# Kernel tuning notes

Hardware: AMD Instinct MI355X
Metric: run time of the kernel (lower is better)

Reference implementation:

```python
import jax, jax.numpy as jnp
import numpy as np

B, C, S, H, W = 2, 192, 16, 32, 32
NH, P = 6, 4          # num_heads, n_points (n_points hardcoded = 4 in source)
HD = C // NH          # head_dim = 32
HID = 4 * C           # mlp hidden (mlp_ratio = 4.0)
L = S * H * W
EPS = 1e-5


def _offset_bias():
    # Faithful to DeformAttention._reset_parameters grid init.
    thetas = np.arange(NH, dtype=np.float32) * (2.0 * np.pi / NH)
    g = np.stack([np.cos(thetas), np.sin(thetas) * np.cos(thetas), np.sin(thetas) * np.sin(thetas)], -1)
    g = g / np.abs(g).max(-1, keepdims=True)
    g = np.tile(g[:, None, :], (1, P, 1)).copy()
    for i in range(P):
        g[:, i, :] *= (i + 1)
    return jnp.asarray(g.reshape(-1), dtype=jnp.float32)


def setup_inputs() -> dict:
    key = jax.random.key(0)
    ks = jax.random.split(key, 8)
    w = lambda k, shp, s: jax.random.normal(k, shp, jnp.float32) * s
    return {
        "x": jax.random.normal(ks[0], (B, C, S, H, W), jnp.float32),
        "mask_matrix": 0,  # unused (shift_size == 0)
        "Wv": w(ks[1], (C, C), C ** -0.5), "bv": jnp.zeros((C,), jnp.float32),
        "Woff": w(ks[2], (C, NH * P * 3), 0.01), "boff": _offset_bias(),
        "Waw": w(ks[3], (C, NH * P), 0.02), "baw": jnp.zeros((NH * P,), jnp.float32),
        "Wout": w(ks[4], (C, C), C ** -0.5), "bout": jnp.zeros((C,), jnp.float32),
        "g2": jnp.ones((C,), jnp.float32), "b2": jnp.zeros((C,), jnp.float32),
        "W1": w(ks[5], (C, HID), C ** -0.5), "b1": jnp.zeros((HID,), jnp.float32),
        "W2": w(ks[6], (HID, C), HID ** -0.5), "b2m": jnp.zeros((C,), jnp.float32),
    }


def _layernorm(x, g, b):
    m = jnp.mean(x, -1, keepdims=True)
    v = jnp.mean(jnp.square(x - m), -1, keepdims=True)
    return (x - m) * jax.lax.rsqrt(v + EPS) * g + b


def _ref_points():
    # get_reference_points with valid_ratios == 1 (mask_ is all-zeros in source).
    d = (jnp.arange(S, dtype=jnp.float32) + 0.5) / S
    y = (jnp.arange(H, dtype=jnp.float32) + 0.5) / H
    x = (jnp.arange(W, dtype=jnp.float32) + 0.5) / W
    rd, ry, rx = jnp.meshgrid(d, y, x, indexing="ij")
    # stacked as (d, x, y), matching normalizer (D, W, H)
    return jnp.stack([rd.reshape(-1), rx.reshape(-1), ry.reshape(-1)], -1)  # (L, 3)


def _deform_core(value, loc, aw):
    # value: (B,L,NH,HD); loc: (B,L,NH,P,3) in [0,1] as (d,x,y); aw: (B,L,NH,P)
    v = value.transpose(0, 2, 1, 3)  # (B,NH,L,HD), L flattened as d*H*W + y*W + x
    pd = loc[..., 0] * S - 0.5  # align_corners=False pixel coords
    px = loc[..., 1] * W - 0.5
    py = loc[..., 2] * H - 0.5
    d0f, x0f, y0f = jnp.floor(pd), jnp.floor(px), jnp.floor(py)
    fd, fx, fy = pd - d0f, px - x0f, py - y0f
    d0, x0, y0 = d0f.astype(jnp.int32), x0f.astype(jnp.int32), y0f.astype(jnp.int32)
    acc = jnp.zeros((B, NH, L * P, HD), value.dtype)
    for dd in (0, 1):
        for dy in (0, 1):
            for dx in (0, 1):
                di, yi, xi = d0 + dd, y0 + dy, x0 + dx
                wgt = (fd if dd else 1.0 - fd) * (fy if dy else 1.0 - fy) * (fx if dx else 1.0 - fx)
                inb = (di >= 0) & (di < S) & (yi >= 0) & (yi < H) & (xi >= 0) & (xi < W)
                idx = (jnp.clip(di, 0, S - 1) * H + jnp.clip(yi, 0, H - 1)) * W + jnp.clip(xi, 0, W - 1)
                idx = idx.transpose(0, 2, 1, 3).reshape(B, NH, L * P)
                samp = jnp.take_along_axis(v, idx[..., None], axis=2)  # (B,NH,L*P,HD)
                wz = jnp.where(inb, wgt, 0.0).transpose(0, 2, 1, 3).reshape(B, NH, L * P, 1)
                acc = acc + samp * wz
    acc = acc.reshape(B, NH, L, P, HD)
    out = jnp.sum(acc * aw.transpose(0, 2, 1, 3)[..., None], axis=3)  # (B,NH,L,HD)
    return out.transpose(0, 2, 1, 3).reshape(B, L, NH * HD)


def reference(x, mask_matrix, Wv, bv, Woff, boff, Waw, baw, Wout, bout, g2, b2, W1, b1, W2, b2m):
    # shortcut = x.view(B, S*H*W, C) on channel-first memory (faithful to source view)
    shortcut = x.reshape(B, L, C)
    xp = x.transpose(0, 2, 3, 4, 1).reshape(B, L, C)  # token-major layout used by attn

    # DeformAttention
    value = (xp @ Wv + bv).reshape(B, L, NH, HD)
    off = (xp @ Woff + boff).reshape(B, L, NH, P, 3)
    aw = jax.nn.softmax((xp @ Waw + baw).reshape(B, L, NH, P), axis=-1)
    norm = jnp.array([S, W, H], jnp.float32)
    loc = _ref_points()[None, :, None, None, :] + off / norm  # (B,L,NH,P,3)
    attn = _deform_core(value, loc, aw) @ Wout + bout  # (B,L,C)

    h = shortcut + attn
    h = h + (jax.nn.gelu(_layernorm(h, g2, b2) @ W1 + b1, approximate=False) @ W2 + b2m)
    return h.reshape(B, S, H, W, C).transpose(0, 4, 1, 2, 3)  # (B,C,S,H,W)
```

## Files before the change

### kernel.cpp

```cpp
#include <hip/hip_runtime.h>
#include <hip/hip_bf16.h>
#include <math.h>

#define BB 2
#define CC 192
#define SS 16
#define HH 32
#define WW 32
#define NH 6
#define PP 4
#define HD 32
#define HID 768
#define LL (SS * HH * WW)
#define MTOK (BB * LL)
#define NPROJ 288

typedef unsigned short u16;
typedef u16 u16x8 __attribute__((ext_vector_type(8)));
typedef __bf16 bf16x8 __attribute__((ext_vector_type(8)));
typedef float f32x4 __attribute__((ext_vector_type(4)));

static __device__ __forceinline__ u16 f2b(float f) {
    __hip_bfloat16 h = __float2bfloat16(f);
    return *reinterpret_cast<u16*>(&h);
}

static __device__ __forceinline__ float fast_gelu(float v) {
    float z = 1.5957691216057308f * (v + 0.044715f * v * v * v);
    return v * __builtin_amdgcn_rcpf(1.0f + __expf(-z));
}

__global__ void build_weights(const float* __restrict__ Wv, const float* __restrict__ Woff,
                              const float* __restrict__ Waw, const float* __restrict__ Wout,
                              const float* __restrict__ W1, const float* __restrict__ W2,
                              const float* __restrict__ bv, const float* __restrict__ boff,
                              const float* __restrict__ baw,
                              u16* __restrict__ wcatT, u16* __restrict__ woutT,
                              u16* __restrict__ w1T, u16* __restrict__ w2T,
                              float* __restrict__ bcat) {
    int i = blockIdx.x * 256 + threadIdx.x;
    if (i < NPROJ * CC) {
        int n = i / CC, k = i % CC;
        float v = (n < 192) ? Wv[k * 192 + n]
                : (n < 264) ? Woff[k * 72 + (n - 192)]
                            : Waw[k * 24 + (n - 264)];
        wcatT[i] = f2b(v);
        return;
    }
    i -= NPROJ * CC;
    if (i < CC * CC) {
        int n = i / CC, k = i % CC;
        woutT[i] = f2b(Wout[k * CC + n]);
        return;
    }
    i -= CC * CC;
    if (i < HID * CC) {
        int n = i / CC, k = i % CC;
        w1T[i] = f2b(W1[k * HID + n]);
        return;
    }
    i -= HID * CC;
    if (i < CC * HID) {
        int n = i / HID, k = i % HID;
        w2T[i] = f2b(W2[k * CC + n]);
        return;
    }
    i -= CC * HID;
    if (i < NPROJ) {
        float v = (i < 192) ? bv[i] : (i < 264) ? boff[i - 192] : baw[i - 264];
        bcat[i] = v;
    }
}

__global__ void transpose_in(const float* __restrict__ x, u16* __restrict__ xp) {
    __shared__ float s[32][33];
    int b = blockIdx.z;
    int c0 = blockIdx.y * 32;
    int l0 = blockIdx.x * 32;
    int tx = threadIdx.x, ty = threadIdx.y;
#pragma unroll
    for (int r = 0; r < 32; r += 8)
        s[ty + r][tx] = x[((size_t)b * CC + c0 + ty + r) * LL + l0 + tx];
    __syncthreads();
#pragma unroll
    for (int r = 0; r < 32; r += 8)
        xp[((size_t)b * LL + l0 + ty + r) * CC + c0 + tx] = f2b(s[tx][ty + r]);
}

template<int EPI, int NF>
__global__ __launch_bounds__(256, 2) void gemm_mfma(const u16* __restrict__ A,
                                                    const u16* __restrict__ Bt,
                                                    const float* __restrict__ bias,
                                                    const float* __restrict__ add,
                                                    void* __restrict__ Cout,
                                                    void* __restrict__ Cout2,
                                                    int M, int N, int K) {
    constexpr int BN = NF * 32;
    __shared__ u16 As[128][40];
    __shared__ u16 Bs[BN][40];
    int t = threadIdx.x;
    int m0 = blockIdx.y * 128;
    int n0 = blockIdx.x * BN;
    int w = t >> 6, lane = t & 63;
    int wm = w >> 1, wn = w & 1;
    int lrow = lane & 15, q = lane >> 4;
    int lk8 = q * 8;

    f32x4 acc[4][NF];
#pragma unroll
    for (int i = 0; i < 4; ++i)
#pragma unroll
        for (int f = 0; f < NF; ++f)
#pragma unroll
            for (int r = 0; r < 4; ++r) acc[i][f][r] = 0.f;

    int arow = t >> 2, aseg = (t & 3) * 8;

    for (int k0 = 0; k0 < K; k0 += 32) {
        *reinterpret_cast<u16x8*>(&As[arow][aseg]) =
            *reinterpret_cast<const u16x8*>(A + (size_t)(m0 + arow) * K + k0 + aseg);
        *reinterpret_cast<u16x8*>(&As[arow + 64][aseg]) =
            *reinterpret_cast<const u16x8*>(A + (size_t)(m0 + arow + 64) * K + k0 + aseg);
#pragma unroll
        for (int idx = 0; idx < BN * 4; idx += 256) {
            int ii = idx + t;
            if (ii < BN * 4) {
                int br = ii >> 2, bseg = (ii & 3) * 8;
                *reinterpret_cast<u16x8*>(&Bs[br][bseg]) =
                    *reinterpret_cast<const u16x8*>(Bt + (size_t)(n0 + br) * K + k0 + bseg);
            }
        }
        __syncthreads();
        bf16x8 af[4], bfr[NF];
#pragma unroll
        for (int i = 0; i < 4; ++i)
            af[i] = *reinterpret_cast<const bf16x8*>(&As[wm * 64 + i * 16 + lrow][lk8]);
#pragma unroll
        for (int f = 0; f < NF; ++f)
            bfr[f] = *reinterpret_cast<const bf16x8*>(&Bs[wn * (16 * NF) + f * 16 + lrow][lk8]);
#pragma unroll
        for (int i = 0; i < 4; ++i)
#pragma unroll
            for (int f = 0; f < NF; ++f) {
                if (EPI == 3)
                    acc[i][f] = __builtin_amdgcn_mfma_f32_16x16x32_bf16(af[i], bfr[f], acc[i][f], 0, 0, 0);
                else
                    acc[i][f] = __builtin_amdgcn_mfma_f32_16x16x32_bf16(bfr[f], af[i], acc[i][f], 0, 0, 0);
            }
        __syncthreads();
    }

    if (EPI == 3) {
#pragma unroll
        for (int i = 0; i < 4; ++i) {
#pragma unroll
            for (int f = 0; f < NF; ++f) {
                int n = n0 + wn * (16 * NF) + f * 16 + lrow;
                float bvn = bias[n];
                int mb = m0 + wm * 64 + i * 16 + q * 4;
                float4 vv;
#pragma unroll
                for (int r = 0; r < 4; ++r)
                    ((float*)&vv)[r] = acc[i][f][r] + bvn + add[(size_t)(mb + r) * N + n];
                int b = mb >> 14, l = mb & (LL - 1);
                *reinterpret_cast<float4*>((float*)Cout + ((size_t)b * CC + n) * LL + l) = vv;
            }
        }
    } else {
#pragma unroll
        for (int i = 0; i < 4; ++i) {
            int m = m0 + wm * 64 + i * 16 + lrow;
#pragma unroll
            for (int f = 0; f < NF; ++f) {
                int nq = n0 + wn * (16 * NF) + f * 16 + q * 4;
                float4 bias4 = *reinterpret_cast<const float4*>(bias + nq);
                if (EPI == 0) {
                    if (nq < 192) {
                        int h = nq >> 5, hd = nq & 31;
                        int b = m >> 14, l = m & (LL - 1);
                        u16 p0 = f2b(acc[i][f][0] + bias4.x);
                        u16 p1 = f2b(acc[i][f][1] + bias4.y);
                        u16 p2 = f2b(acc[i][f][2] + bias4.z);
                        u16 p3 = f2b(acc[i][f][3] + bias4.w);
                        uint2 pk = make_uint2((unsigned)p0 | ((unsigned)p1 << 16),
                                              (unsigned)p2 | ((unsigned)p3 << 16));
                        *reinterpret_cast<uint2*>(
                            (u16*)Cout + (((size_t)b * NH + h) * LL + l) * HD + hd) = pk;
                    } else {
                        float4 vv;
                        vv.x = acc[i][f][0] + bias4.x;
                        vv.y = acc[i][f][1] + bias4.y;
                        vv.z = acc[i][f][2] + bias4.z;
                        vv.w = acc[i][f][3] + bias4.w;
                        *reinterpret_cast<float4*>((float*)Cout2 + (size_t)m * 96 + (nq - 192)) = vv;
                    }
                } else if (EPI == 1) {
                    float4 add4 = *reinterpret_cast<const float4*>(add + (size_t)m * N + nq);
                    float4 vv;
                    vv.x = acc[i][f][0] + bias4.x + add4.x;
                    vv.y = acc[i][f][1] + bias4.y + add4.y;
                    vv.z = acc[i][f][2] + bias4.z + add4.z;
                    vv.w = acc[i][f][3] + bias4.w + add4.w;
                    *reinterpret_cast<float4*>((float*)Cout + (size_t)m * N + nq) = vv;
                } else {
                    u16 p0 = f2b(fast_gelu(acc[i][f][0] + bias4.x));
                    u16 p1 = f2b(fast_gelu(acc[i][f][1] + bias4.y));
                    u16 p2 = f2b(fast_gelu(acc[i][f][2] + bias4.z));
                    u16 p3 = f2b(fast_gelu(acc[i][f][3] + bias4.w));
                    uint2 pk = make_uint2((unsigned)p0 | ((unsigned)p1 << 16),
                                          (unsigned)p2 | ((unsigned)p3 << 16));
                    *reinterpret_cast<uint2*>((u16*)Cout + (size_t)m * N + nq) = pk;
                }
            }
        }
    }
}

__global__ __launch_bounds__(256) void deform_kernel(const u16* __restrict__ vbuf,
                                                     const float* __restrict__ offaw,
                                                     u16* __restrict__ dout) {
    __shared__ uint2 cw[8][32];
    int gl = threadIdx.x >> 5;
    int g = blockIdx.x * 8 + gl;
    int j = threadIdx.x & 31;
    int h = g % NH;
    int tmp = g / NH;
    int l = tmp % LL;
    int b = tmp / LL;
    int d = l >> 10, rem = l & 1023, y = rem >> 5, xw = rem & 31;

    const float* oa = offaw + (size_t)(b * LL + l) * 96;
    int p = j >> 3, cor = j & 7;
    int dx = cor & 1, dy = (cor >> 1) & 1, dd = cor >> 2;

    float4 lg = *reinterpret_cast<const float4*>(oa + 72 + h * 4);
    float mx = fmaxf(fmaxf(lg.x, lg.y), fmaxf(lg.z, lg.w));
    float e0 = __expf(lg.x - mx), e1 = __expf(lg.y - mx);
    float e2 = __expf(lg.z - mx), e3 = __expf(lg.w - mx);
    float inv = __builtin_amdgcn_rcpf(e0 + e1 + e2 + e3);
    float ep = (p == 0) ? e0 : (p == 1) ? e1 : (p == 2) ? e2 : e3;
    float awp = ep * inv;

    const float* op = oa + (h * 4 + p) * 3;
    float pd = (d + 0.5f) + op[0] - 0.5f;
    float px = (xw + 0.5f) + op[1] - 0.5f;
    float py = (y + 0.5f) + op[2] - 0.5f;
    float d0f = floorf(pd), x0f = floorf(px), y0f = floorf(py);
    float fd = pd - d0f, fx = px - x0f, fy = py - y0f;
    int di = (int)d0f + dd, yi = (int)y0f + dy, xi = (int)x0f + dx;
    bool inb = (di >= 0) & (di < SS) & (yi >= 0) & (yi < HH) & (xi >= 0) & (xi < WW);
    float wgt = (dd ? fd : 1.f - fd) * (dy ? fy : 1.f - fy) * (dx ? fx : 1.f - fx) * awp;
    wgt = inb ? wgt : 0.f;
    int dic = min(max(di, 0), SS - 1);
    int yic = min(max(yi, 0), HH - 1);
    int xic = min(max(xi, 0), WW - 1);
    int bo = (((dic * HH) + yic) * WW + xic) * (HD * 2);

    cw[gl][j] = make_uint2((unsigned)bo, __float_as_uint(wgt));
    __syncthreads();

    const char* vhead = (const char*)(vbuf + ((size_t)(b * NH + h) * LL) * HD) + 2 * j;
    const uint4* cw4 = reinterpret_cast<const uint4*>(&cw[gl][0]);
    float acc = 0.f;
#pragma unroll
    for (int qq = 0; qq < 16; ++qq) {
        uint4 c = cw4[qq];
        u16 v0 = *reinterpret_cast<const u16*>(vhead + c.x);
        u16 v1 = *reinterpret_cast<const u16*>(vhead + c.z);
        acc += __uint_as_float(c.y) * __uint_as_float(((unsigned)v0) << 16);
        acc += __uint_as_float(c.w) * __uint_as_float(((unsigned)v1) << 16);
    }
    dout[(size_t)(b * LL + l) * CC + h * HD + j] = f2b(acc);
}

__global__ __launch_bounds__(256) void layernorm_kernel(const float* __restrict__ hin,
                                                        const float* __restrict__ g2,
                                                        const float* __restrict__ b2,
                                                        u16* __restrict__ lnout) {
    int row = blockIdx.x * 4 + (threadIdx.x >> 6);
    int lane = threadIdx.x & 63;
    const float* hr = hin + (size_t)row * CC;
    float v0 = hr[lane], v1 = hr[lane + 64], v2 = hr[lane + 128];
    float s = v0 + v1 + v2;
    float sq = v0 * v0 + v1 * v1 + v2 * v2;
#pragma unroll
    for (int o = 32; o > 0; o >>= 1) {
        s += __shfl_xor(s, o);
        sq += __shfl_xor(sq, o);
    }
    float m = s * (1.0f / CC);
    float var = sq * (1.0f / CC) - m * m;
    float r = rsqrtf(var + 1e-5f);
    u16* lo = lnout + (size_t)row * CC;
    lo[lane]       = f2b((v0 - m) * r * g2[lane]       + b2[lane]);
    lo[lane + 64]  = f2b((v1 - m) * r * g2[lane + 64]  + b2[lane + 64]);
    lo[lane + 128] = f2b((v2 - m) * r * g2[lane + 128] + b2[lane + 128]);
}

extern "C" void kernel_launch(void* const* d_in, const int* in_sizes, int n_in,
                              void* d_out, int out_size, void* d_ws, size_t ws_size,
                              hipStream_t stream) {
    const float* x    = (const float*)d_in[0];
    const float* Wv   = (const float*)d_in[2];
    const float* bv   = (const float*)d_in[3];
    const float* Woff = (const float*)d_in[4];
    const float* boff = (const float*)d_in[5];
    const float* Waw  = (const float*)d_in[6];
    const float* baw  = (const float*)d_in[7];
    const float* Wout = (const float*)d_in[8];
    const float* bout = (const float*)d_in[9];
    const float* g2   = (const float*)d_in[10];
    const float* b2   = (const float*)d_in[11];
    const float* W1   = (const float*)d_in[12];
    const float* b1   = (const float*)d_in[13];
    const float* W2   = (const float*)d_in[14];
    const float* b2m  = (const float*)d_in[15];

    char* wsb = (char*)d_ws;
    u16*   xp    = (u16*)(wsb + 0);
    u16*   vbuf  = (u16*)(wsb + 12582912);
    float* offaw = (float*)(wsb + 25165824);
    u16*   dbuf  = (u16*)(wsb + 0);
    u16*   hid   = (u16*)(wsb + 12582912);
    float* hbuf  = (float*)(wsb + 66060288);
    u16*   ln    = (u16*)(wsb + 92274688);
    u16*   wcatT = (u16*)(wsb + 105906176);
    u16*   woutT = wcatT + NPROJ * CC;
    u16*   w1T   = woutT + CC * CC;
    u16*   w2T   = w1T + HID * CC;
    float* bcat  = (float*)(w2T + CC * HID);
    float* out   = (float*)d_out;

    int wtot = NPROJ * CC + CC * CC + HID * CC + CC * HID + NPROJ;
    build_weights<<<(wtot + 255) / 256, 256, 0, stream>>>(
        Wv, Woff, Waw, Wout, W1, W2, bv, boff, baw, wcatT, woutT, w1T, w2T, bcat);
    transpose_in<<<dim3(LL / 32, CC / 32, BB), dim3(32, 8), 0, stream>>>(x, xp);
    gemm_mfma<0, 3><<<dim3(3, MTOK / 128), 256, 0, stream>>>(
        xp, wcatT, bcat, nullptr, vbuf, offaw, MTOK, NPROJ, CC);
    deform_kernel<<<(BB * LL * NH) / 8, 256, 0, stream>>>(vbuf, offaw, dbuf);
    gemm_mfma<1, 3><<<dim3(2, MTOK / 128), 256, 0, stream>>>(
        dbuf, woutT, bout, x , hbuf, nullptr, MTOK, CC, CC);
    layernorm_kernel<<<MTOK / 4, 256, 0, stream>>>(hbuf, g2, b2, ln);
    gemm_mfma<2, 6><<<dim3(4, MTOK / 128), 256, 0, stream>>>(
        ln, w1T, b1, nullptr, hid, nullptr, MTOK, HID, CC);
    gemm_mfma<3, 3><<<dim3(2, MTOK / 128), 256, 0, stream>>>(
        hid, w2T, b2m, hbuf, out, nullptr, MTOK, CC, HID);
}
```

Before: 265.2 us.

## Double-buffer GEMM LDS tiles and split deform gather into paired-channel halves

The MFMA GEMM now uses two LDS buffers. The next K-tile's global loads are issued into registers before computing on the current tile, which overlaps memory latency with MFMA work and removes one barrier per iteration. In the deformable sampling kernel, each thread loads 32-bit pairs of bf16 channels over half the sample corners. The two halves are combined with a shuffle and written as packed pairs, halving gather instruction count. LDS use per GEMM block doubles, which may hurt occupancy, and the shuffle assumes the halves sit within a wavefront.

```diff
diff --git a/kernel.cpp b/kernel.cpp
--- a/kernel.cpp
+++ b/kernel.cpp
@@ -96,8 +96,9 @@
                                                     void* __restrict__ Cout2,
                                                     int M, int N, int K) {
     constexpr int BN = NF * 32;
-    __shared__ u16 As[128][40];
-    __shared__ u16 Bs[BN][40];
+    constexpr int NB = (BN * 4 + 255) / 256;
+    __shared__ u16 As[2][128][40];
+    __shared__ u16 Bs[2][BN][40];
     int t = threadIdx.x;
     int m0 = blockIdx.y * 128;
     int n0 = blockIdx.x * BN;
@@ -115,29 +116,85 @@
             for (int r = 0; r < 4; ++r) acc[i][f][r] = 0.f;
 
     int arow = t >> 2, aseg = (t & 3) * 8;
-
-    for (int k0 = 0; k0 < K; k0 += 32) {
-        *reinterpret_cast<u16x8*>(&As[arow][aseg]) =
-            *reinterpret_cast<const u16x8*>(A + (size_t)(m0 + arow) * K + k0 + aseg);
-        *reinterpret_cast<u16x8*>(&As[arow + 64][aseg]) =
-            *reinterpret_cast<const u16x8*>(A + (size_t)(m0 + arow + 64) * K + k0 + aseg);
-#pragma unroll
-        for (int idx = 0; idx < BN * 4; idx += 256) {
-            int ii = idx + t;
+    const u16* Arow0 = A + (size_t)(m0 + arow) * K + aseg;
+    const u16* Arow1 = A + (size_t)(m0 + arow + 64) * K + aseg;
+
+    u16x8 av0, av1, bv[NB];
+    av0 = *reinterpret_cast<const u16x8*>(Arow0);
+    av1 = *reinterpret_cast<const u16x8*>(Arow1);
+#pragma unroll
+    for (int u2 = 0; u2 < NB; ++u2) {
+        int ii = t + u2 * 256;
+        if (ii < BN * 4) {
+            int br = ii >> 2, bseg = (ii & 3) * 8;
+            bv[u2] = *reinterpret_cast<const u16x8*>(Bt + (size_t)(n0 + br) * K + bseg);
+        }
+    }
+    *reinterpret_cast<u16x8*>(&As[0][arow][aseg]) = av0;
+    *reinterpret_cast<u16x8*>(&As[0][arow + 64][aseg]) = av1;
+#pragma unroll
+    for (int u2 = 0; u2 < NB; ++u2) {
+        int ii = t + u2 * 256;
+        if (ii < BN * 4) {
+            int br = ii >> 2, bseg = (ii & 3) * 8;
+            *reinterpret_cast<u16x8*>(&Bs[0][br][bseg]) = bv[u2];
+        }
+    }
+    __syncthreads();
+
+    int NT = K >> 5;
+    int cur = 0;
+    for (int ti = 0; ti < NT - 1; ++ti) {
+        int k1 = (ti + 1) << 5;
+        av0 = *reinterpret_cast<const u16x8*>(Arow0 + k1);
+        av1 = *reinterpret_cast<const u16x8*>(Arow1 + k1);
+#pragma unroll
+        for (int u2 = 0; u2 < NB; ++u2) {
+            int ii = t + u2 * 256;
             if (ii < BN * 4) {
                 int br = ii >> 2, bseg = (ii & 3) * 8;
-                *reinterpret_cast<u16x8*>(&Bs[br][bseg]) =
-                    *reinterpret_cast<const u16x8*>(Bt + (size_t)(n0 + br) * K + k0 + bseg);
+                bv[u2] = *reinterpret_cast<const u16x8*>(Bt + (size_t)(n0 + br) * K + k1 + bseg);
             }
         }
+        {
+            bf16x8 af[4], bfr[NF];
+#pragma unroll
+            for (int i = 0; i < 4; ++i)
+                af[i] = *reinterpret_cast<const bf16x8*>(&As[cur][wm * 64 + i * 16 + lrow][lk8]);
+#pragma unroll
+            for (int f = 0; f < NF; ++f)
+                bfr[f] = *reinterpret_cast<const bf16x8*>(&Bs[cur][wn * (16 * NF) + f * 16 + lrow][lk8]);
+#pragma unroll
+            for (int i = 0; i < 4; ++i)
+#pragma unroll
+                for (int f = 0; f < NF; ++f) {
+                    if (EPI == 3)
+                        acc[i][f] = __builtin_amdgcn_mfma_f32_16x16x32_bf16(af[i], bfr[f], acc[i][f], 0, 0, 0);
+                    else
+                        acc[i][f] = __builtin_amdgcn_mfma_f32_16x16x32_bf16(bfr[f], af[i], acc[i][f], 0, 0, 0);
+                }
+        }
+        *reinterpret_cast<u16x8*>(&As[cur ^ 1][arow][aseg]) = av0;
+        *reinterpret_cast<u16x8*>(&As[cur ^ 1][arow + 64][aseg]) = av1;
+#pragma unroll
+        for (int u2 = 0; u2 < NB; ++u2) {
+            int ii = t + u2 * 256;
+            if (ii < BN * 4) {
+                int br = ii >> 2, bseg = (ii & 3) * 8;
+                *reinterpret_cast<u16x8*>(&Bs[cur ^ 1][br][bseg]) = bv[u2];
+            }
+        }
         __syncthreads();
+        cur ^= 1;
+    }
+    {
         bf16x8 af[4], bfr[NF];
 #pragma unroll
         for (int i = 0; i < 4; ++i)
-            af[i] = *reinterpret_cast<const bf16x8*>(&As[wm * 64 + i * 16 + lrow][lk8]);
+            af[i] = *reinterpret_cast<const bf16x8*>(&As[cur][wm * 64 + i * 16 + lrow][lk8]);
 #pragma unroll
         for (int f = 0; f < NF; ++f)
-            bfr[f] = *reinterpret_cast<const bf16x8*>(&Bs[wn * (16 * NF) + f * 16 + lrow][lk8]);
+            bfr[f] = *reinterpret_cast<const bf16x8*>(&Bs[cur][wn * (16 * NF) + f * 16 + lrow][lk8]);
 #pragma unroll
         for (int i = 0; i < 4; ++i)
 #pragma unroll
@@ -147,7 +204,6 @@
                 else
                     acc[i][f] = __builtin_amdgcn_mfma_f32_16x16x32_bf16(bfr[f], af[i], acc[i][f], 0, 0, 0);
             }
-        __syncthreads();
     }
 
     if (EPI == 3) {
@@ -259,18 +315,27 @@
     cw[gl][j] = make_uint2((unsigned)bo, __float_as_uint(wgt));
     __syncthreads();
 
-    const char* vhead = (const char*)(vbuf + ((size_t)(b * NH + h) * LL) * HD) + 2 * j;
-    const uint4* cw4 = reinterpret_cast<const uint4*>(&cw[gl][0]);
-    float acc = 0.f;
-#pragma unroll
-    for (int qq = 0; qq < 16; ++qq) {
+    int half = j >> 4, jc = j & 15;
+    const char* vbase2 = (const char*)(vbuf + ((size_t)(b * NH + h) * LL) * HD) + 4 * jc;
+    const uint4* cw4 = reinterpret_cast<const uint4*>(&cw[gl][half * 16]);
+    float a0 = 0.f, a1 = 0.f;
+#pragma unroll
+    for (int qq = 0; qq < 8; ++qq) {
         uint4 c = cw4[qq];
-        u16 v0 = *reinterpret_cast<const u16*>(vhead + c.x);
-        u16 v1 = *reinterpret_cast<const u16*>(vhead + c.z);
-        acc += __uint_as_float(c.y) * __uint_as_float(((unsigned)v0) << 16);
-        acc += __uint_as_float(c.w) * __uint_as_float(((unsigned)v1) << 16);
-    }
-    dout[(size_t)(b * LL + l) * CC + h * HD + j] = f2b(acc);
+        unsigned u0 = *reinterpret_cast<const unsigned*>(vbase2 + c.x);
+        unsigned u1 = *reinterpret_cast<const unsigned*>(vbase2 + c.z);
+        float w0 = __uint_as_float(c.y), w1 = __uint_as_float(c.w);
+        a0 += w0 * __uint_as_float(u0 << 16);
+        a1 += w0 * __uint_as_float(u0 & 0xffff0000u);
+        a0 += w1 * __uint_as_float(u1 << 16);
+        a1 += w1 * __uint_as_float(u1 & 0xffff0000u);
+    }
+    a0 += __shfl_xor(a0, 16);
+    a1 += __shfl_xor(a1, 16);
+    if (half == 0) {
+        unsigned pk = (unsigned)f2b(a0) | ((unsigned)f2b(a1) << 16);
+        *reinterpret_cast<unsigned*>(dout + (size_t)(b * LL + l) * CC + h * HD + 2 * jc) = pk;
+    }
 }
 
 __global__ __launch_bounds__(256) void layernorm_kernel(const float* __restrict__ hin,
```

After: 228.0 us. 14.0% less time.
